# Kernel optimization log

Measured on AMD Instinct MI355X. Metric: run time of the kernel, lower is better.

## Reference

```python
import jax, jax.numpy as jnp
import numpy as np

EMBED_DIM = 128
N_EMBED = 10000
INPUT_SHAPE = (8, 64, 32, EMBED_DIM)


def setup_inputs() -> dict:
    key = jax.random.key(0)
    k1, k2 = jax.random.split(key)
    inputs = jax.random.normal(k1, INPUT_SHAPE, dtype=jnp.float32)
    cluster_mean = jax.random.normal(k2, (EMBED_DIM, N_EMBED), dtype=jnp.float32)
    return {"inputs": inputs, "cluster_mean": cluster_mean}


def reference(inputs, cluster_mean):
    embed_dim = cluster_mean.shape[0]
    # Flatten all leading dims: (N, D)
    samples = inputs.reshape(-1, embed_dim)
    # Squared euclidean distance to each code: (N, n_embed)
    dist = (
        jnp.sum(samples ** 2, axis=1, keepdims=True)
        - 2.0 * samples @ cluster_mean
        + jnp.sum(cluster_mean ** 2, axis=0, keepdims=True)
    )
    cluster_index = jnp.argmin(dist, axis=1).reshape(inputs.shape[:-1])
    # Embedding lookup from transposed codebook: (..., D)
    quantize = cluster_mean.T[cluster_index]
    q_loss = jnp.mean((quantize - jax.lax.stop_gradient(inputs)) ** 2)
    e_loss = jnp.mean((jax.lax.stop_gradient(quantize) - inputs) ** 2)
    loss = q_loss + 0.25 * e_loss
    # Straight-through estimator
    outputs = inputs + jax.lax.stop_gradient(quantize - inputs)
    return outputs, loss
```

## Files before the change

kernel.cpp:

```cpp
#include <hip/hip_runtime.h>

#define EMBED 128
#define NCODE 10000
#define NSAMP 16384
#define NCODE_PAD 10240
#define NSPLIT 8
#define SPLIT_CODES 1280
#define NCHUNK 20
#define CHUNK_ELEMS 8192
#define OUT_ELEMS (NSAMP * EMBED)
#define TAU 0.002f
#define NSEG 16

typedef float f32x16 __attribute__((ext_vector_type(16)));
typedef short s16x8 __attribute__((ext_vector_type(8)));
typedef unsigned short ushort_t;
typedef unsigned long long u64;

#define OFF_AH  0
#define OFF_AL  2621440
#define OFF_CT  5242880
#define OFF_CN  10485760
#define OFF_KEY 10526720
#define OFF_C2  11575296
#define OFF_IDX 12099584
#define OFF_RL  12165120
#define OFF_CNT 12230656
#define OFF_BEST 12230720

__device__ __forceinline__ unsigned short f2bf(float f) {
    unsigned u = __float_as_uint(f);
    return (unsigned short)((u + 0x7fffu + ((u >> 16) & 1u)) >> 16);
}
__device__ __forceinline__ float bf2f(unsigned short h) {
    return __uint_as_float(((unsigned)h) << 16);
}
__device__ __forceinline__ unsigned ordf(float f) {
    unsigned u = __float_as_uint(f);
    return (u & 0x80000000u) ? ~u : (u | 0x80000000u);
}
__device__ __forceinline__ float unordf(unsigned o) {
    return __uint_as_float((o & 0x80000000u) ? (o ^ 0x80000000u) : ~o);
}

__global__ __launch_bounds__(256) void prep_norm(const float* __restrict__ C,
                                                 float* __restrict__ cnorm,
                                                 float* __restrict__ out,
                                                 int* __restrict__ counter) {
    int j = blockIdx.x * 256 + threadIdx.x;
    if (j == 0) { out[OUT_ELEMS] = 0.f; *counter = 0; }
    if (j >= NCODE_PAD) return;
    if (j >= NCODE) { cnorm[j] = 3.0e38f; return; }
    float s = 0.f;
#pragma unroll 8
    for (int d = 0; d < EMBED; ++d) {
        float v = C[d * NCODE + j];
        s = fmaf(v, v, s);
    }
    cnorm[j] = s;
}

__global__ __launch_bounds__(256) void prep_c4(const float* __restrict__ C,
                                               ushort_t* __restrict__ Ah,
                                               ushort_t* __restrict__ Al,
                                               float* __restrict__ CT) {
    int o = blockIdx.x * 256 + threadIdx.x;
    int n  = o % NCODE_PAD;
    int kg = o / NCODE_PAD;
    int split = n / SPLIT_CODES;
    int rem   = n % SPLIT_CODES;
    int chunk = rem >> 6;
    int mb    = (rem >> 5) & 1;
    int row   = rem & 31;
    int ks = kg >> 1, kh = kg & 1;
    size_t eoff = (size_t)(split * NCHUNK + chunk) * CHUNK_ELEMS
                + (size_t)(mb * 4096 + (ks * 2 + kh) * 256 + row * 8);
    int k0 = kg * 8;
    float f[8];
#pragma unroll
    for (int j = 0; j < 8; ++j)
        f[j] = (n < NCODE) ? C[(size_t)(k0 + j) * NCODE + n] : 0.f;
    *(float4*)(CT + (size_t)n * EMBED + k0)     = make_float4(f[0], f[1], f[2], f[3]);
    *(float4*)(CT + (size_t)n * EMBED + k0 + 4) = make_float4(f[4], f[5], f[6], f[7]);
    s16x8 vh, vl;
#pragma unroll
    for (int j = 0; j < 8; ++j) {
        unsigned short h = f2bf(f[j]);
        vh[j] = (short)h;
        vl[j] = (short)f2bf(f[j] - bf2f(h));
    }
    *(s16x8*)(Ah + eoff) = vh;
    *(s16x8*)(Al + eoff) = vl;
}

__global__ __launch_bounds__(256, 2) void vq7(const float* __restrict__ X,
                                              const ushort_t* __restrict__ Ah,
                                              const ushort_t* __restrict__ Al,
                                              const float* __restrict__ cnorm,
                                              u64* __restrict__ candKey,
                                              unsigned* __restrict__ cand2) {
    __shared__ ushort_t Bs[2 * 2 * CHUNK_ELEMS];
    const int t    = threadIdx.x;
    const int lane = t & 63;
    const int wave = t >> 6;
    const int ln   = lane & 31;
    const int kh   = lane >> 5;
    const int split = blockIdx.y;
    const int m0    = blockIdx.x * 256;

    s16x8 bh[2][8], bl[2][8];
#pragma unroll
    for (int g = 0; g < 2; ++g) {
        int m = m0 + wave * 64 + g * 32 + ln;
#pragma unroll
        for (int ks = 0; ks < 8; ++ks) {
            const float* src = X + (size_t)m * EMBED + ks * 16 + kh * 8;
            float4 f0 = *(const float4*)src;
            float4 f1 = *(const float4*)(src + 4);
            float f[8] = {f0.x, f0.y, f0.z, f0.w, f1.x, f1.y, f1.z, f1.w};
            s16x8 vh, vl;
#pragma unroll
            for (int j = 0; j < 8; ++j) {
                float v = -2.f * f[j];
                unsigned short h = f2bf(v);
                vh[j] = (short)h;
                vl[j] = (short)f2bf(v - bf2f(h));
            }
            bh[g][ks] = vh;
            bl[g][ks] = vl;
        }
    }

    float v1[2] = {3.4e38f, 3.4e38f}, v2[2] = {3.4e38f, 3.4e38f};
    int   j1[2] = {0, 0};

    auto ldsw = (__attribute__((address_space(3))) ushort_t*)Bs;
    const int woff = wave * 2048;
    const size_t chbase = (size_t)(split * NCHUNK) * CHUNK_ELEMS;

    {
        const ushort_t* sh = Ah + chbase + woff + lane * 8;
        const ushort_t* sl = Al + chbase + woff + lane * 8;
#pragma unroll
        for (int i = 0; i < 4; ++i) {
            __builtin_amdgcn_global_load_lds(
                (const __attribute__((address_space(1))) void*)(sh + i * 512),
                (__attribute__((address_space(3))) void*)(ldsw + woff + i * 512),
                16, 0, 0);
            __builtin_amdgcn_global_load_lds(
                (const __attribute__((address_space(1))) void*)(sl + i * 512),
                (__attribute__((address_space(3))) void*)(ldsw + CHUNK_ELEMS + woff + i * 512),
                16, 0, 0);
        }
    }
    __syncthreads();

    for (int c = 0; c < NCHUNK; ++c) {
        const int b = c & 1;
        if (c + 1 < NCHUNK) {
            const size_t sb = chbase + (size_t)(c + 1) * CHUNK_ELEMS;
            const ushort_t* sh = Ah + sb + woff + lane * 8;
            const ushort_t* sl = Al + sb + woff + lane * 8;
            const int db = (1 - b) * 2 * CHUNK_ELEMS + woff;
#pragma unroll
            for (int i = 0; i < 4; ++i) {
                __builtin_amdgcn_global_load_lds(
                    (const __attribute__((address_space(1))) void*)(sh + i * 512),
                    (__attribute__((address_space(3))) void*)(ldsw + db + i * 512),
                    16, 0, 0);
                __builtin_amdgcn_global_load_lds(
                    (const __attribute__((address_space(1))) void*)(sl + i * 512),
                    (__attribute__((address_space(3))) void*)(ldsw + db + CHUNK_ELEMS + i * 512),
                    16, 0, 0);
            }
        }

        const int bb = b * 2 * CHUNK_ELEMS;
        const int cbase = split * SPLIT_CODES + c * 64 + 4 * kh;

#pragma unroll
        for (int mb = 0; mb < 2; ++mb) {
            f32x16 acc0 = {0,0,0,0,0,0,0,0,0,0,0,0,0,0,0,0};
            f32x16 acc1 = {0,0,0,0,0,0,0,0,0,0,0,0,0,0,0,0};
#pragma unroll
            for (int ks = 0; ks < 8; ++ks) {
                const int fo = bb + mb * 4096 + (ks * 2 + kh) * 256 + ln * 8;
                s16x8 a_h = *(const s16x8*)&Bs[fo];
                s16x8 a_l = *(const s16x8*)&Bs[CHUNK_ELEMS + fo];
                acc0 = __builtin_amdgcn_mfma_f32_32x32x16_bf16(a_h, bh[0][ks], acc0, 0, 0, 0);
                acc1 = __builtin_amdgcn_mfma_f32_32x32x16_bf16(a_h, bh[1][ks], acc1, 0, 0, 0);
                acc0 = __builtin_amdgcn_mfma_f32_32x32x16_bf16(a_h, bl[0][ks], acc0, 0, 0, 0);
                acc1 = __builtin_amdgcn_mfma_f32_32x32x16_bf16(a_h, bl[1][ks], acc1, 0, 0, 0);
                acc0 = __builtin_amdgcn_mfma_f32_32x32x16_bf16(a_l, bh[0][ks], acc0, 0, 0, 0);
                acc1 = __builtin_amdgcn_mfma_f32_32x32x16_bf16(a_l, bh[1][ks], acc1, 0, 0, 0);
            }
#pragma unroll
            for (int r = 0; r < 16; ++r) {
                const int code = cbase + mb * 32 + ((r & 3) + 8 * (r >> 2));
                const float cn = cnorm[code];
                float d;
                d = acc0[r] + cn;
                if (d < v1[0]) { v2[0] = v1[0]; v1[0] = d; j1[0] = code; }
                else           { v2[0] = fminf(v2[0], d); }
                d = acc1[r] + cn;
                if (d < v1[1]) { v2[1] = v1[1]; v1[1] = d; j1[1] = code; }
                else           { v2[1] = fminf(v2[1], d); }
            }
        }
        __syncthreads();
    }

#pragma unroll
    for (int g = 0; g < 2; ++g) {
        float ov1 = __shfl_xor(v1[g], 32, 64);
        int   oj1 = __shfl_xor(j1[g], 32, 64);
        float ov2 = __shfl_xor(v2[g], 32, 64);
        float hi = fmaxf(v1[g], ov1);
        v2[g] = fminf(fminf(v2[g], ov2), hi);
        if (ov1 < v1[g] || (ov1 == v1[g] && oj1 < j1[g])) { v1[g] = ov1; j1[g] = oj1; }
        if (kh == 0) {
            int m = m0 + wave * 64 + g * 32 + ln;
            candKey[(size_t)m * NSPLIT + split] =
                ((u64)ordf(v1[g]) << 32) | (unsigned)j1[g];
            cand2[(size_t)m * NSPLIT + split] = ordf(v2[g]);
        }
    }
}

__global__ __launch_bounds__(256) void outfin_k(const float* __restrict__ X,
                                                const float* __restrict__ CT,
                                                const u64* __restrict__ candKey,
                                                const unsigned* __restrict__ cand2,
                                                int* __restrict__ idxf,
                                                int* __restrict__ rlist,
                                                int* __restrict__ counter,
                                                u64* __restrict__ wsBest,
                                                float* __restrict__ out) {
    __shared__ float red[4];
    const int t = threadIdx.x;
    const int m = blockIdx.x * 8 + (t >> 5);
    const int l = t & 31;

    int code = 0;
    if (l == 0) {
        u64 best = 0xffffffffffffffffull;
        float v2 = 3.4e38f;
#pragma unroll
        for (int s = 0; s < NSPLIT; ++s) {
            u64 k = candKey[(size_t)m * NSPLIT + s];
            unsigned o2 = cand2[(size_t)m * NSPLIT + s];
            if (k < best) {
                if (best != 0xffffffffffffffffull)
                    v2 = fminf(v2, unordf((unsigned)(best >> 32)));
                best = k;
                v2 = fminf(v2, unordf(o2));
            } else {
                v2 = fminf(v2, unordf((unsigned)(k >> 32)));
            }
        }
        code = (int)(unsigned)(best & 0xffffffffu);
        idxf[m] = code;
        float v1 = unordf((unsigned)(best >> 32));
        if (v2 - v1 <= TAU) {
            rlist[atomicAdd(counter, 1)] = m;
            wsBest[m] = 0xffffffffffffffffull;
        }
    }
    code = __shfl(code, 0, 32);

    float4 q = *(const float4*)(CT + (size_t)code * EMBED + l * 4);
    float4 x = *(const float4*)(X + (size_t)m * EMBED + l * 4);
    *(float4*)(out + (size_t)m * EMBED + l * 4) = q;
    float dx = q.x - x.x, dy = q.y - x.y, dz = q.z - x.z, dw = q.w - x.w;
    float lsum = dx * dx + dy * dy + dz * dz + dw * dw;
#pragma unroll
    for (int off = 1; off < 64; off <<= 1) lsum += __shfl_xor(lsum, off, 64);
    if ((t & 63) == 0) red[t >> 6] = lsum;
    __syncthreads();
    if (t == 0)
        atomicAdd(out + OUT_ELEMS,
                  (red[0] + red[1] + red[2] + red[3]) * (1.25f / (float)OUT_ELEMS));
}

__global__ __launch_bounds__(256) void rescue_seg(const float* __restrict__ X,
                                                  const float* __restrict__ CT,
                                                  const float* __restrict__ cnorm,
                                                  const int* __restrict__ rlist,
                                                  const int* __restrict__ counter,
                                                  u64* __restrict__ wsBest) {
    __shared__ float xs[EMBED];
    __shared__ u64 wk[4];
    const int t = threadIdx.x;
    const int lane = t & 63;
    const int wave = t >> 6;
    const int hw = t & 31;
    const int slot = t >> 5;
    const int cnt = *counter;
    const int nw = cnt * NSEG;

    for (int w = blockIdx.x; w < nw; w += gridDim.x) {
        const int s = w >> 4, seg = w & 15;
        const int m = rlist[s];
        __syncthreads();
        if (t < 32) {
            float4 v = *(const float4*)(X + (size_t)m * EMBED + t * 4);
            xs[t * 4 + 0] = v.x; xs[t * 4 + 1] = v.y;
            xs[t * 4 + 2] = v.z; xs[t * 4 + 3] = v.w;
        }
        __syncthreads();
        const float x0 = xs[hw * 4 + 0], x1 = xs[hw * 4 + 1];
        const float x2 = xs[hw * 4 + 2], x3 = xs[hw * 4 + 3];
        const int base = seg * 625;
        const int jend = base + 625;
        u64 bk = 0xffffffffffffffffull;
        for (int it = 0; it < 20; ++it) {
            const int r0 = base + it * 32 + slot * 4;
            float4 c0, c1, c2, c3;
            bool ok0 = (r0 + 0 < jend), ok1 = (r0 + 1 < jend);
            bool ok2 = (r0 + 2 < jend), ok3 = (r0 + 3 < jend);
            c0 = ok0 ? *(const float4*)(CT + (size_t)(r0 + 0) * EMBED + hw * 4) : make_float4(0, 0, 0, 0);
            c1 = ok1 ? *(const float4*)(CT + (size_t)(r0 + 1) * EMBED + hw * 4) : make_float4(0, 0, 0, 0);
            c2 = ok2 ? *(const float4*)(CT + (size_t)(r0 + 2) * EMBED + hw * 4) : make_float4(0, 0, 0, 0);
            c3 = ok3 ? *(const float4*)(CT + (size_t)(r0 + 3) * EMBED + hw * 4) : make_float4(0, 0, 0, 0);
            float p0 = x0 * c0.x, p1 = x0 * c1.x, p2 = x0 * c2.x, p3 = x0 * c3.x;
            p0 = fmaf(x1, c0.y, p0); p1 = fmaf(x1, c1.y, p1);
            p2 = fmaf(x1, c2.y, p2); p3 = fmaf(x1, c3.y, p3);
            p0 = fmaf(x2, c0.z, p0); p1 = fmaf(x2, c1.z, p1);
            p2 = fmaf(x2, c2.z, p2); p3 = fmaf(x2, c3.z, p3);
            p0 = fmaf(x3, c0.w, p0); p1 = fmaf(x3, c1.w, p1);
            p2 = fmaf(x3, c2.w, p2); p3 = fmaf(x3, c3.w, p3);
#pragma unroll
            for (int off = 1; off < 32; off <<= 1) {
                p0 += __shfl_xor(p0, off, 32);
                p1 += __shfl_xor(p1, off, 32);
                p2 += __shfl_xor(p2, off, 32);
                p3 += __shfl_xor(p3, off, 32);
            }
            if (hw == 0) {
                if (ok0) { u64 k = ((u64)ordf(fmaf(-2.f, p0, cnorm[r0 + 0])) << 32) | (unsigned)(r0 + 0); if (k < bk) bk = k; }
                if (ok1) { u64 k = ((u64)ordf(fmaf(-2.f, p1, cnorm[r0 + 1])) << 32) | (unsigned)(r0 + 1); if (k < bk) bk = k; }
                if (ok2) { u64 k = ((u64)ordf(fmaf(-2.f, p2, cnorm[r0 + 2])) << 32) | (unsigned)(r0 + 2); if (k < bk) bk = k; }
                if (ok3) { u64 k = ((u64)ordf(fmaf(-2.f, p3, cnorm[r0 + 3])) << 32) | (unsigned)(r0 + 3); if (k < bk) bk = k; }
            }
        }
#pragma unroll
        for (int off = 1; off < 64; off <<= 1) {
            u64 o = __shfl_xor(bk, off, 64);
            if (o < bk) bk = o;
        }
        if (lane == 0) wk[wave] = bk;
        __syncthreads();
        if (t == 0) {
            u64 b = wk[0];
            if (wk[1] < b) b = wk[1];
            if (wk[2] < b) b = wk[2];
            if (wk[3] < b) b = wk[3];
            atomicMin(&wsBest[m], b);
        }
    }
}

__global__ __launch_bounds__(256) void patch_k(const float* __restrict__ X,
                                               const float* __restrict__ CT,
                                               const int* __restrict__ rlist,
                                               const int* __restrict__ counter,
                                               const u64* __restrict__ wsBest,
                                               const int* __restrict__ idxf,
                                               float* __restrict__ out) {
    const int t = threadIdx.x;
    const int l = t & 31, sl = t >> 5;
    const int cnt = *counter;
    for (int s = blockIdx.x * 8 + sl; s < cnt; s += gridDim.x * 8) {
        int m = rlist[s];
        u64 key = wsBest[m];
        int jn = (int)(unsigned)(key & 0xffffffffu);
        int jo = idxf[m];
        if (jn == jo) continue;
        float4 qn = *(const float4*)(CT + (size_t)jn * EMBED + l * 4);
        float4 qo = *(const float4*)(CT + (size_t)jo * EMBED + l * 4);
        float4 x  = *(const float4*)(X + (size_t)m * EMBED + l * 4);
        *(float4*)(out + (size_t)m * EMBED + l * 4) = qn;
        float dn = (qn.x - x.x) * (qn.x - x.x) + (qn.y - x.y) * (qn.y - x.y)
                 + (qn.z - x.z) * (qn.z - x.z) + (qn.w - x.w) * (qn.w - x.w);
        float dp = (qo.x - x.x) * (qo.x - x.x) + (qo.y - x.y) * (qo.y - x.y)
                 + (qo.z - x.z) * (qo.z - x.z) + (qo.w - x.w) * (qo.w - x.w);
        float delta = dn - dp;
#pragma unroll
        for (int off = 1; off < 32; off <<= 1) delta += __shfl_xor(delta, off, 32);
        if (l == 0)
            atomicAdd(out + OUT_ELEMS, delta * (1.25f / (float)OUT_ELEMS));
    }
}

extern "C" void kernel_launch(void* const* d_in, const int* in_sizes, int n_in,
                              void* d_out, int out_size, void* d_ws, size_t ws_size,
                              hipStream_t stream) {
    const float* X = (const float*)d_in[0];
    const float* C = (const float*)d_in[1];
    float* out = (float*)d_out;
    char* ws = (char*)d_ws;

    ushort_t* Ah = (ushort_t*)(ws + OFF_AH);
    ushort_t* Al = (ushort_t*)(ws + OFF_AL);
    float* CT    = (float*)(ws + OFF_CT);
    float* cnorm = (float*)(ws + OFF_CN);
    u64* candKey = (u64*)(ws + OFF_KEY);
    unsigned* cand2 = (unsigned*)(ws + OFF_C2);
    int* idxf    = (int*)(ws + OFF_IDX);
    int* rlist   = (int*)(ws + OFF_RL);
    int* counter = (int*)(ws + OFF_CNT);
    u64* wsBest  = (u64*)(ws + OFF_BEST);

    prep_norm<<<NCODE_PAD / 256, 256, 0, stream>>>(C, cnorm, out, counter);
    prep_c4<<<(NCODE_PAD * 16) / 256, 256, 0, stream>>>(C, Ah, Al, CT);
    vq7<<<dim3(NSAMP / 256, NSPLIT), 256, 0, stream>>>(X, Ah, Al, cnorm, candKey, cand2);
    outfin_k<<<NSAMP / 8, 256, 0, stream>>>(X, CT, candKey, cand2, idxf, rlist, counter, wsBest, out);
    rescue_seg<<<1024, 256, 0, stream>>>(X, CT, cnorm, rlist, counter, wsBest);
    patch_k<<<64, 256, 0, stream>>>(X, CT, rlist, counter, wsBest, idxf, out);
}
```

Baseline: 263.6 us.

## Triple-buffer codebook chunks in 512-thread blocks with finer waitcnt sync

The main distance kernel moves to 512-thread blocks (8 waves, 512 samples per block), which halves the codebook staging work each wave does and spreads the reuse of each loaded chunk over twice as many samples. The LDS ring grows from two to three buffers so chunks are prefetched two iterations ahead. The full __syncthreads is replaced by an explicit vmcnt wait plus s_barrier, MFMA sections are raised in priority with s_setprio, and the code norms for the split are cached in LDS. The goal is to hide global-to-LDS latency and cut barrier stalls, at the cost of more LDS per block and possibly lower occupancy with 512 threads and 2 blocks per CU.

```diff
diff --git a/kernel.cpp b/kernel.cpp
--- a/kernel.cpp
+++ b/kernel.cpp
@@ -93,20 +93,22 @@
     *(s16x8*)(Al + eoff) = vl;
 }
 
-__global__ __launch_bounds__(256, 2) void vq7(const float* __restrict__ X,
+__global__ __launch_bounds__(512, 2) void vq7(const float* __restrict__ X,
                                               const ushort_t* __restrict__ Ah,
                                               const ushort_t* __restrict__ Al,
                                               const float* __restrict__ cnorm,
                                               u64* __restrict__ candKey,
                                               unsigned* __restrict__ cand2) {
-    __shared__ ushort_t Bs[2 * 2 * CHUNK_ELEMS];
+    __shared__ ushort_t Bs[3 * 2 * CHUNK_ELEMS];
+    __shared__ float cns[SPLIT_CODES];
     const int t    = threadIdx.x;
     const int lane = t & 63;
     const int wave = t >> 6;
     const int ln   = lane & 31;
     const int kh   = lane >> 5;
     const int split = blockIdx.y;
-    const int m0    = blockIdx.x * 256;
+    const int m0    = blockIdx.x * 512;
+    const int sbase = split * SPLIT_CODES;
 
     s16x8 bh[2][8], bl[2][8];
 #pragma unroll
@@ -131,57 +133,52 @@
         }
     }
 
+    for (int i = t; i < SPLIT_CODES; i += 512) cns[i] = cnorm[sbase + i];
+
     float v1[2] = {3.4e38f, 3.4e38f}, v2[2] = {3.4e38f, 3.4e38f};
     int   j1[2] = {0, 0};
 
     auto ldsw = (__attribute__((address_space(3))) ushort_t*)Bs;
-    const int woff = wave * 2048;
+    const int woff = wave * 1024;
     const size_t chbase = (size_t)(split * NCHUNK) * CHUNK_ELEMS;
 
-    {
-        const ushort_t* sh = Ah + chbase + woff + lane * 8;
-        const ushort_t* sl = Al + chbase + woff + lane * 8;
-#pragma unroll
-        for (int i = 0; i < 4; ++i) {
+    auto stage = [&](int cc, int buf) {
+        const size_t sb = chbase + (size_t)cc * CHUNK_ELEMS;
+        const ushort_t* sh = Ah + sb + woff + lane * 8;
+        const ushort_t* sl = Al + sb + woff + lane * 8;
+        const int db = buf * 2 * CHUNK_ELEMS + woff;
+#pragma unroll
+        for (int i = 0; i < 2; ++i) {
             __builtin_amdgcn_global_load_lds(
                 (const __attribute__((address_space(1))) void*)(sh + i * 512),
-                (__attribute__((address_space(3))) void*)(ldsw + woff + i * 512),
+                (__attribute__((address_space(3))) void*)(ldsw + db + i * 512),
                 16, 0, 0);
             __builtin_amdgcn_global_load_lds(
                 (const __attribute__((address_space(1))) void*)(sl + i * 512),
-                (__attribute__((address_space(3))) void*)(ldsw + CHUNK_ELEMS + woff + i * 512),
+                (__attribute__((address_space(3))) void*)(ldsw + db + CHUNK_ELEMS + i * 512),
                 16, 0, 0);
         }
-    }
+    };
+
+    stage(0, 0);
+    stage(1, 1);
     __syncthreads();
 
+    int b = 0;
     for (int c = 0; c < NCHUNK; ++c) {
-        const int b = c & 1;
-        if (c + 1 < NCHUNK) {
-            const size_t sb = chbase + (size_t)(c + 1) * CHUNK_ELEMS;
-            const ushort_t* sh = Ah + sb + woff + lane * 8;
-            const ushort_t* sl = Al + sb + woff + lane * 8;
-            const int db = (1 - b) * 2 * CHUNK_ELEMS + woff;
-#pragma unroll
-            for (int i = 0; i < 4; ++i) {
-                __builtin_amdgcn_global_load_lds(
-                    (const __attribute__((address_space(1))) void*)(sh + i * 512),
-                    (__attribute__((address_space(3))) void*)(ldsw + db + i * 512),
-                    16, 0, 0);
-                __builtin_amdgcn_global_load_lds(
-                    (const __attribute__((address_space(1))) void*)(sl + i * 512),
-                    (__attribute__((address_space(3))) void*)(ldsw + db + CHUNK_ELEMS + i * 512),
-                    16, 0, 0);
-            }
+        if (c + 2 < NCHUNK) {
+            int nb = b + 2; if (nb >= 3) nb -= 3;
+            stage(c + 2, nb);
         }
 
         const int bb = b * 2 * CHUNK_ELEMS;
-        const int cbase = split * SPLIT_CODES + c * 64 + 4 * kh;
+        const int cb = c * 64 + 4 * kh;
 
 #pragma unroll
         for (int mb = 0; mb < 2; ++mb) {
             f32x16 acc0 = {0,0,0,0,0,0,0,0,0,0,0,0,0,0,0,0};
             f32x16 acc1 = {0,0,0,0,0,0,0,0,0,0,0,0,0,0,0,0};
+            __builtin_amdgcn_s_setprio(1);
 #pragma unroll
             for (int ks = 0; ks < 8; ++ks) {
                 const int fo = bb + mb * 4096 + (ks * 2 + kh) * 256 + ln * 8;
@@ -194,10 +191,12 @@
                 acc0 = __builtin_amdgcn_mfma_f32_32x32x16_bf16(a_l, bh[0][ks], acc0, 0, 0, 0);
                 acc1 = __builtin_amdgcn_mfma_f32_32x32x16_bf16(a_l, bh[1][ks], acc1, 0, 0, 0);
             }
+            __builtin_amdgcn_s_setprio(0);
 #pragma unroll
             for (int r = 0; r < 16; ++r) {
-                const int code = cbase + mb * 32 + ((r & 3) + 8 * (r >> 2));
-                const float cn = cnorm[code];
+                const int cc = cb + mb * 32 + ((r & 3) + 8 * (r >> 2));
+                const float cn = cns[cc];
+                const int code = sbase + cc;
                 float d;
                 d = acc0[r] + cn;
                 if (d < v1[0]) { v2[0] = v1[0]; v1[0] = d; j1[0] = code; }
@@ -207,7 +206,11 @@
                 else           { v2[1] = fminf(v2[1], d); }
             }
         }
-        __syncthreads();
+
+        if (c < NCHUNK - 2) asm volatile("s_waitcnt vmcnt(4)" ::: "memory");
+        else                asm volatile("s_waitcnt vmcnt(0)" ::: "memory");
+        asm volatile("s_barrier" ::: "memory");
+        ++b; if (b >= 3) b = 0;
     }
 
 #pragma unroll
@@ -413,7 +416,7 @@
 
     prep_norm<<<NCODE_PAD / 256, 256, 0, stream>>>(C, cnorm, out, counter);
     prep_c4<<<(NCODE_PAD * 16) / 256, 256, 0, stream>>>(C, Ah, Al, CT);
-    vq7<<<dim3(NSAMP / 256, NSPLIT), 256, 0, stream>>>(X, Ah, Al, cnorm, candKey, cand2);
+    vq7<<<dim3(NSAMP / 512, NSPLIT), 512, 0, stream>>>(X, Ah, Al, cnorm, candKey, cand2);
     outfin_k<<<NSAMP / 8, 256, 0, stream>>>(X, CT, candKey, cand2, idxf, rlist, counter, wsBest, out);
     rescue_seg<<<1024, 256, 0, stream>>>(X, CT, cnorm, rlist, counter, wsBest);
     patch_k<<<64, 256, 0, stream>>>(X, CT, rlist, counter, wsBest, idxf, out);
```

Measured after the change: 258.1 us. 1.02x faster.
